# Kernel tuning notes

Measured on AMD Instinct MI355X. Metric: run time of the kernel, lower is better.

The kernel has to match this reference:

```python
import jax, jax.numpy as jnp
import numpy as np

B, T, I, H = 64, 512, 1024, 1024


def setup_inputs() -> dict:
    key = jax.random.key(0)
    ks = jax.random.split(key, 8)
    s = 0.02
    return {
        "x": jax.random.normal(ks[0], (B, T, I), dtype=jnp.float32),
        "h_0": jax.random.normal(ks[1], (B, H), dtype=jnp.float32),
        "W_ih": jax.random.normal(ks[2], (H, I), dtype=jnp.float32) * s,
        "b_ih": jax.random.normal(ks[3], (H,), dtype=jnp.float32) * s,
        "W_hh1": jax.random.normal(ks[4], (H, H), dtype=jnp.float32) * s,
        "b_hh1": jax.random.normal(ks[5], (H,), dtype=jnp.float32) * s,
        "W_hh2": jax.random.normal(ks[6], (H, H), dtype=jnp.float32) * s,
        "b_hh2": jax.random.normal(ks[7], (H,), dtype=jnp.float32) * s,
    }


def reference(x, h_0, W_ih, b_ih, W_hh1, b_hh1, W_hh2, b_hh2):
    # Shared input projection is time-independent: hoist out of the scan.
    # xp: [B, T, H]
    xp = jnp.einsum("bti,hi->bth", x, W_ih) + b_ih

    def step(h, xp_t):
        # xp_t: [B, H], h: [B, H]
        v1 = jnp.tanh(xp_t + h @ W_hh1.T + b_hh1)
        v2 = jnp.tanh(xp_t + h @ W_hh2.T + b_hh2)
        h_new = (1.0 - h) * v1 + h * v2
        return h_new, h_new

    h_T, ys = jax.lax.scan(step, h_0, jnp.swapaxes(xp, 0, 1))  # ys: [T, B, H]
    out = jnp.swapaxes(ys, 0, 1)  # [B, T, H]
    # nn.Dropout is identity in eval mode; reference is deterministic.
    return out, h_T
```

## Files before the change

kernel.cpp:

```cpp
#include <hip/hip_runtime.h>

using u32 = unsigned int;
using u64 = unsigned long long;
using bf16x8 = __attribute__((ext_vector_type(8))) short;
using f32x4  = __attribute__((ext_vector_type(4))) float;

#define BB_ 64
#define TT_ 512
#define II_ 1024
#define HH_ 1024
#define NSCAN_BLOCKS 128

__device__ __forceinline__ unsigned short bf16rne(float f) {
  u32 u = __float_as_uint(f);
  return (unsigned short)((u + 0x7FFFu + ((u >> 16) & 1u)) >> 16);
}
__device__ __forceinline__ u32 pk2(float a, float b) {
  u32 ua = __float_as_uint(a), ub = __float_as_uint(b);
  u32 lo = (ua + 0x7FFFu + ((ua >> 16) & 1u)) >> 16;
  u32 hi = (ub + 0x7FFFu + ((ub >> 16) & 1u)) & 0xFFFF0000u;
  return lo | hi;
}
__device__ __forceinline__ void gll16(const void* g, void* s) {
  __builtin_amdgcn_global_load_lds(
      (const __attribute__((address_space(1))) u32*)g,
      (__attribute__((address_space(3))) u32*)s, 16, 0, 0);
}
__device__ __forceinline__ float tanhfast(float x) {
  float e = __builtin_amdgcn_exp2f(x * 2.885390081777927f);
  return 1.0f - 2.0f / (e + 1.0f);
}

__device__ __forceinline__ void cvt4(const float* __restrict__ s, unsigned short* __restrict__ d, long long g) {
  float4 v = ((const float4*)s)[g];
  ushort4 o;
  o.x = bf16rne(v.x); o.y = bf16rne(v.y); o.z = bf16rne(v.z); o.w = bf16rne(v.w);
  ((ushort4*)d)[g] = o;
}

__global__ void k_convert(const float* __restrict__ x, const float* __restrict__ h0,
                          const float* __restrict__ Wih, const float* __restrict__ Wh1,
                          const float* __restrict__ Wh2,
                          unsigned short* __restrict__ xb, unsigned short* __restrict__ Wihb,
                          unsigned short* __restrict__ Wcatb, unsigned short* __restrict__ hbuf,
                          int* __restrict__ cnt, int do_x) {
  const long long NWI = (long long)HH_ * II_ / 4;
  const long long NH0 = (long long)BB_ * HH_ / 4;
  const long long NC  = 1024;
  const long long NX  = do_x ? ((long long)BB_ * TT_ * II_ / 4) : 0;
  const long long total = 3 * NWI + NH0 + NC + NX;
  for (long long g = (long long)blockIdx.x * blockDim.x + threadIdx.x; g < total;
       g += (long long)gridDim.x * blockDim.x) {
    if (g < NWI) {
      cvt4(Wih, Wihb, g);
    } else if (g < 2 * NWI) {
      cvt4(Wh1, Wcatb, g - NWI);
    } else if (g < 3 * NWI) {
      cvt4(Wh2, Wcatb + (long long)HH_ * II_, g - 2 * NWI);
    } else if (g < 3 * NWI + NH0) {
      cvt4(h0, hbuf, g - 3 * NWI);
    } else if (g < 3 * NWI + NH0 + NC) {
      ((int4*)cnt)[g - 3 * NWI - NH0] = make_int4(0, 0, 0, 0);
    } else {
      cvt4(x, xb, g - (3 * NWI + NH0 + NC));
    }
  }
}

template <bool XB>
__global__ __launch_bounds__(256) void k_gemm(const unsigned short* __restrict__ xbg,
                                              const float* __restrict__ xf,
                                              const unsigned short* __restrict__ Wb,
                                              const float* __restrict__ bias,
                                              float* __restrict__ C) {
  __shared__ __align__(16) unsigned short ldsA[128 * 64];
  __shared__ __align__(16) unsigned short ldsB[128 * 64];
  const int tid = threadIdx.x;
  const int w = tid >> 6, l = tid & 63;
  const int lr = l & 15, lk = l >> 4;
  const int n0 = (blockIdx.x & 7) * 128;
  const int m0 = (blockIdx.x >> 3) * 128;
  const int mbase = (w >> 1) * 64, nbase = (w & 1) * 64;

  f32x4 acc[4][4] = {};

  for (int kb = 0; kb < 16; ++kb) {
    const int k0 = kb * 64;
#pragma unroll
    for (int r = 0; r < 4; ++r) {
      int tb = r * 4096 + w * 1024 + l * 16;
      int row = tb >> 7;
      int p = (tb >> 4) & 7;
      int c = p ^ (row & 7);
      gll16(Wb + (u64)(n0 + row) * II_ + k0 + c * 8,
            (char*)ldsB + r * 4096 + w * 1024);
    }
    if constexpr (XB) {
#pragma unroll
      for (int r = 0; r < 4; ++r) {
        int tb = r * 4096 + w * 1024 + l * 16;
        int row = tb >> 7;
        int p = (tb >> 4) & 7;
        int c = p ^ (row & 7);
        gll16(xbg + (u64)(m0 + row) * II_ + k0 + c * 8,
              (char*)ldsA + r * 4096 + w * 1024);
      }
    } else {
      const int r = tid >> 1, ch = tid & 1;
      const float* gs = xf + (u64)(m0 + r) * II_ + k0 + ch * 32;
      float4 v[8];
#pragma unroll
      for (int q = 0; q < 8; ++q) v[q] = ((const float4*)gs)[q];
#pragma unroll
      for (int q = 0; q < 4; ++q) {
        int c = ch * 4 + q;
        int p = c ^ (r & 7);
        uint4 pk;
        pk.x = pk2(v[2 * q].x, v[2 * q].y);
        pk.y = pk2(v[2 * q].z, v[2 * q].w);
        pk.z = pk2(v[2 * q + 1].x, v[2 * q + 1].y);
        pk.w = pk2(v[2 * q + 1].z, v[2 * q + 1].w);
        *(uint4*)((char*)ldsA + r * 128 + p * 16) = pk;
      }
    }
    __syncthreads();

    bf16x8 a[4][2], b[4][2];
#pragma unroll
    for (int mt = 0; mt < 4; ++mt) {
      int row = mbase + mt * 16 + lr;
#pragma unroll
      for (int kk = 0; kk < 2; ++kk) {
        int c = kk * 4 + lk, p = c ^ (row & 7);
        a[mt][kk] = *(const bf16x8*)((const char*)ldsA + row * 128 + p * 16);
      }
    }
#pragma unroll
    for (int nt = 0; nt < 4; ++nt) {
      int row = nbase + nt * 16 + lr;
#pragma unroll
      for (int kk = 0; kk < 2; ++kk) {
        int c = kk * 4 + lk, p = c ^ (row & 7);
        b[nt][kk] = *(const bf16x8*)((const char*)ldsB + row * 128 + p * 16);
      }
    }
#pragma unroll
    for (int kk = 0; kk < 2; ++kk)
#pragma unroll
      for (int mt = 0; mt < 4; ++mt)
#pragma unroll
        for (int nt = 0; nt < 4; ++nt)
          acc[mt][nt] = __builtin_amdgcn_mfma_f32_16x16x32_bf16(a[mt][kk], b[nt][kk], acc[mt][nt], 0, 0, 0);
    __syncthreads();
  }

  float bn[4];
#pragma unroll
  for (int nt = 0; nt < 4; ++nt) bn[nt] = bias[n0 + nbase + nt * 16 + lr];
#pragma unroll
  for (int mt = 0; mt < 4; ++mt) {
#pragma unroll
    for (int i = 0; i < 4; ++i) {
      int m = m0 + mbase + mt * 16 + lk * 4 + i;
      float* cr = C + (u64)m * HH_ + n0 + nbase + lr;
#pragma unroll
      for (int nt = 0; nt < 4; ++nt) cr[nt * 16] = acc[mt][nt][i] + bn[nt];
    }
  }
}

__global__ __launch_bounds__(256, 1) void k_scan(float* __restrict__ out, const float* __restrict__ h0,
                                                 const float* __restrict__ b1, const float* __restrict__ b2,
                                                 const unsigned short* __restrict__ Wcat,
                                                 unsigned short* __restrict__ hbuf, u32* __restrict__ flags) {
  __shared__ float part[16 * 4 * 65];
  const int tid = threadIdx.x, w = tid >> 6, l = tid & 63;
  const int lr = l & 15, lk = l >> 4;
  const int og = blockIdx.x & 31, bg = blockIdx.x >> 5;
  const int jb = og * 32, bb = bg * 16;
  const int koff = w * 256;

  bf16x8 wt[4][8];
#pragma unroll
  for (int nt = 0; nt < 4; ++nt) {
    int nrow = (nt < 2) ? (jb + nt * 16 + lr) : (HH_ + jb + (nt - 2) * 16 + lr);
    const unsigned short* wr = Wcat + (u64)nrow * HH_ + koff + lk * 8;
#pragma unroll
    for (int kk = 0; kk < 8; ++kk) wt[nt][kk] = *(const bf16x8*)(wr + kk * 32);
  }

  const int b = tid & 15, jp = tid >> 4;
  const int grow = bb + b;
  const int c0 = jb + jp * 2;
  float bv1[2] = {b1[c0], b1[c0 + 1]};
  float bv2[2] = {b2[c0], b2[c0 + 1]};
  float hold[2] = {h0[(u64)grow * HH_ + c0], h0[(u64)grow * HH_ + c0 + 1]};
  float* outp = out + (u64)grow * TT_ * HH_ + c0;

  u32* dflag = flags + bg * 512;
  const u64 ldw = ((u64)(bb + lr) * HH_ + koff + lk * 8) >> 2;
  const u64 stw = ((u64)grow * HH_ + c0) >> 1;

  for (int t = 0; t < TT_; ++t) {
    float2 xpv = *(const float2*)(outp + (u64)t * HH_);

    if (t > 0) {
      if (w == 0) {
        const u32 need = (u32)t;
        while (true) {
          u32 v = (l < 32)
                      ? __hip_atomic_load(dflag + l * 16, __ATOMIC_RELAXED, __HIP_MEMORY_SCOPE_AGENT)
                      : 0xFFFFFFFFu;
          if (__all((int)(v >= need))) break;
        }
      }
      __syncthreads();
    }

    const u64* hB = (const u64*)hbuf + (u64)(t & 1) * (BB_ * HH_ / 4) + ldw;
    bf16x8 av[8];
#pragma unroll
    for (int kk = 0; kk < 8; ++kk) {
      union { u64 q[2]; bf16x8 v; } au;
      au.q[0] = __hip_atomic_load(hB + kk * 8,     __ATOMIC_RELAXED, __HIP_MEMORY_SCOPE_AGENT);
      au.q[1] = __hip_atomic_load(hB + kk * 8 + 1, __ATOMIC_RELAXED, __HIP_MEMORY_SCOPE_AGENT);
      av[kk] = au.v;
    }

    f32x4 acc[4] = {};
#pragma unroll
    for (int kk = 0; kk < 8; ++kk)
#pragma unroll
      for (int nt = 0; nt < 4; ++nt)
        asm("v_mfma_f32_16x16x32_bf16 %0, %1, %2, %0"
            : "+v"(acc[nt]) : "v"(av[kk]), "a"(wt[nt][kk]));
    asm volatile("s_nop 7\n\ts_nop 7\n\ts_nop 7"
                 : "+v"(acc[0]), "+v"(acc[1]), "+v"(acc[2]), "+v"(acc[3]));

#pragma unroll
    for (int nt = 0; nt < 4; ++nt)
#pragma unroll
      for (int i = 0; i < 4; ++i)
        part[((w * 4 + nt) * 4 + i) * 65 + l] = acc[nt][i];
    __syncthreads();

    float hn[2];
#pragma unroll
    for (int q = 0; q < 2; ++q) {
      const int cl = jp * 2 + q;
      const int nt1 = cl >> 4, jl = cl & 15;
      const int lidx = (b >> 2) * 16 + jl, ridx = b & 3;
      float v1 = 0.f, v2 = 0.f;
#pragma unroll
      for (int ww = 0; ww < 4; ++ww) {
        v1 += part[((ww * 4 + nt1) * 4 + ridx) * 65 + lidx];
        v2 += part[((ww * 4 + 2 + nt1) * 4 + ridx) * 65 + lidx];
      }
      float xi = (q == 0) ? xpv.x : xpv.y;
      float t1 = tanhfast(v1 + xi + bv1[q]);
      float t2 = tanhfast(v2 + xi + bv2[q]);
      hn[q] = t1 + hold[q] * (t2 - t1);
      hold[q] = hn[q];
    }

    if (t < TT_ - 1) {
      u32 wd = (u32)bf16rne(hn[0]) | ((u32)bf16rne(hn[1]) << 16);
      __hip_atomic_store((u32*)hbuf + (u64)((t + 1) & 1) * (BB_ * HH_ / 2) + stw, wd,
                         __ATOMIC_RELAXED, __HIP_MEMORY_SCOPE_AGENT);
      asm volatile("s_waitcnt vmcnt(0)" ::: "memory");
      __syncthreads();
      if (tid == 0)
        __hip_atomic_store(dflag + og * 16, (u32)(t + 1), __ATOMIC_RELAXED, __HIP_MEMORY_SCOPE_AGENT);
    } else {
      *(float2*)(out + (u64)BB_ * TT_ * HH_ + (u64)grow * HH_ + c0) = make_float2(hn[0], hn[1]);
    }

    *(float2*)(outp + (u64)t * HH_) = make_float2(hn[0], hn[1]);
  }
}

extern "C" void kernel_launch(void* const* d_in, const int* in_sizes, int n_in,
                              void* d_out, int out_size, void* d_ws, size_t ws_size,
                              hipStream_t stream) {
  const float* x    = (const float*)d_in[0];
  const float* h0   = (const float*)d_in[1];
  const float* Wih  = (const float*)d_in[2];
  const float* bih  = (const float*)d_in[3];
  const float* Whh1 = (const float*)d_in[4];
  const float* bhh1 = (const float*)d_in[5];
  const float* Whh2 = (const float*)d_in[6];
  const float* bhh2 = (const float*)d_in[7];
  float* out = (float*)d_out;

  char* ws = (char*)d_ws;
  unsigned short* Wihb  = (unsigned short*)(ws + 0);
  unsigned short* Wcatb = (unsigned short*)(ws + 2097152);
  unsigned short* hbuf  = (unsigned short*)(ws + 6291456);
  int*            cnt   = (int*)(ws + 6553600);
  unsigned short* xb    = (unsigned short*)(ws + 6569984);
  const bool fastx = ws_size >= 73678848ULL;

  hipLaunchKernelGGL(k_convert, dim3(2048), dim3(256), 0, stream,
                     x, h0, Wih, Whh1, Whh2, xb, Wihb, Wcatb, hbuf, cnt, (int)fastx);
  if (fastx)
    hipLaunchKernelGGL((k_gemm<true>), dim3(2048), dim3(256), 0, stream,
                       xb, (const float*)nullptr, Wihb, bih, out);
  else
    hipLaunchKernelGGL((k_gemm<false>), dim3(2048), dim3(256), 0, stream,
                       (const unsigned short*)nullptr, x, Wihb, bih, out);
  hipLaunchKernelGGL(k_scan, dim3(NSCAN_BLOCKS), dim3(256), 0, stream,
                     out, h0, bhh1, bhh2, Wcatb, hbuf, (u32*)cnt);
}
```

Measured before the change: 2.187 ms.

## Fuse input-projection GEMM and recurrent scan into one persistent kernel with chunk flags

Merges the input-projection GEMM and the sequential scan into one launch. The first 128 blocks run the scan and the rest run GEMM tiles, which are reordered so that time chunks of 128 steps finish in order. Each finished tile bumps a per-chunk counter, and scan blocks spin on that counter before consuming a chunk, so the recurrence can start while later projections are still being computed. The separate bf16 conversion of x is dropped in favour of converting fp32 x inside the GEMM. The risk is that GEMM blocks compete with scan blocks for compute units and memory bandwidth, and that correctness depends on the scan blocks being resident first.

Measured after the change: 2.270 ms. 3.8% more time.

```diff
diff --git a/kernel.cpp b/kernel.cpp
--- a/kernel.cpp
+++ b/kernel.cpp
@@ -9,7 +9,9 @@
 #define TT_ 512
 #define II_ 1024
 #define HH_ 1024
-#define NSCAN_BLOCKS 128
+#define SCAN_BLOCKS 128
+#define GEMM_BLOCKS 2048
+#define XP_PER_CHUNK 512u
 
 __device__ __forceinline__ unsigned short bf16rne(float f) {
   u32 u = __float_as_uint(f);
@@ -38,17 +40,16 @@
   ((ushort4*)d)[g] = o;
 }
 
-__global__ void k_convert(const float* __restrict__ x, const float* __restrict__ h0,
+__global__ void k_convert(const float* __restrict__ h0,
                           const float* __restrict__ Wih, const float* __restrict__ Wh1,
                           const float* __restrict__ Wh2,
-                          unsigned short* __restrict__ xb, unsigned short* __restrict__ Wihb,
+                          unsigned short* __restrict__ Wihb,
                           unsigned short* __restrict__ Wcatb, unsigned short* __restrict__ hbuf,
-                          int* __restrict__ cnt, int do_x) {
+                          int* __restrict__ cnt) {
   const long long NWI = (long long)HH_ * II_ / 4;
   const long long NH0 = (long long)BB_ * HH_ / 4;
   const long long NC  = 1024;
-  const long long NX  = do_x ? ((long long)BB_ * TT_ * II_ / 4) : 0;
-  const long long total = 3 * NWI + NH0 + NC + NX;
+  const long long total = 3 * NWI + NH0 + NC;
   for (long long g = (long long)blockIdx.x * blockDim.x + threadIdx.x; g < total;
        g += (long long)gridDim.x * blockDim.x) {
     if (g < NWI) {
@@ -59,27 +60,26 @@
       cvt4(Wh2, Wcatb + (long long)HH_ * II_, g - 2 * NWI);
     } else if (g < 3 * NWI + NH0) {
       cvt4(h0, hbuf, g - 3 * NWI);
-    } else if (g < 3 * NWI + NH0 + NC) {
+    } else {
       ((int4*)cnt)[g - 3 * NWI - NH0] = make_int4(0, 0, 0, 0);
-    } else {
-      cvt4(x, xb, g - (3 * NWI + NH0 + NC));
-    }
-  }
-}
-
-template <bool XB>
-__global__ __launch_bounds__(256) void k_gemm(const unsigned short* __restrict__ xbg,
-                                              const float* __restrict__ xf,
-                                              const unsigned short* __restrict__ Wb,
-                                              const float* __restrict__ bias,
-                                              float* __restrict__ C) {
-  __shared__ __align__(16) unsigned short ldsA[128 * 64];
-  __shared__ __align__(16) unsigned short ldsB[128 * 64];
+    }
+  }
+}
+
+__device__ void gemm_role(int gb, char* smem, const float* __restrict__ xf,
+                          const unsigned short* __restrict__ Wb,
+                          const float* __restrict__ bias, float* __restrict__ C,
+                          u32* __restrict__ cnt_xp) {
+  unsigned short* ldsA = (unsigned short*)smem;
+  unsigned short* ldsB = (unsigned short*)(smem + 16384);
   const int tid = threadIdx.x;
   const int w = tid >> 6, l = tid & 63;
   const int lr = l & 15, lk = l >> 4;
-  const int n0 = (blockIdx.x & 7) * 128;
-  const int m0 = (blockIdx.x >> 3) * 128;
+  const int tile = gb >> 3;
+  const int n0 = (gb & 7) * 128;
+  const int tq = tile >> 6;
+  const int bidx = tile & 63;
+  const int m0 = (bidx * 4 + tq) * 128;
   const int mbase = (w >> 1) * 64, nbase = (w & 1) * 64;
 
   f32x4 acc[4][4] = {};
@@ -95,17 +95,7 @@
       gll16(Wb + (u64)(n0 + row) * II_ + k0 + c * 8,
             (char*)ldsB + r * 4096 + w * 1024);
     }
-    if constexpr (XB) {
-#pragma unroll
-      for (int r = 0; r < 4; ++r) {
-        int tb = r * 4096 + w * 1024 + l * 16;
-        int row = tb >> 7;
-        int p = (tb >> 4) & 7;
-        int c = p ^ (row & 7);
-        gll16(xbg + (u64)(m0 + row) * II_ + k0 + c * 8,
-              (char*)ldsA + r * 4096 + w * 1024);
-      }
-    } else {
+    {
       const int r = tid >> 1, ch = tid & 1;
       const float* gs = xf + (u64)(m0 + r) * II_ + k0 + ch * 32;
       float4 v[8];
@@ -167,16 +157,23 @@
       for (int nt = 0; nt < 4; ++nt) cr[nt * 16] = acc[mt][nt][i] + bn[nt];
     }
   }
-}
-
-__global__ __launch_bounds__(256, 1) void k_scan(float* __restrict__ out, const float* __restrict__ h0,
-                                                 const float* __restrict__ b1, const float* __restrict__ b2,
-                                                 const unsigned short* __restrict__ Wcat,
-                                                 unsigned short* __restrict__ hbuf, u32* __restrict__ flags) {
-  __shared__ float part[16 * 4 * 65];
+
+  asm volatile("s_waitcnt vmcnt(0)" ::: "memory");
+  __syncthreads();
+  if (tid == 0)
+    __hip_atomic_fetch_add(cnt_xp + tq, 1u, __ATOMIC_RELEASE, __HIP_MEMORY_SCOPE_AGENT);
+}
+
+__device__ void scan_role(int sb, char* smem, float* __restrict__ out,
+                          const float* __restrict__ h0,
+                          const float* __restrict__ b1, const float* __restrict__ b2,
+                          const unsigned short* __restrict__ Wcat,
+                          unsigned short* __restrict__ hbuf, u32* __restrict__ flags,
+                          u32* __restrict__ cnt_xp) {
+  float* part = (float*)smem;
   const int tid = threadIdx.x, w = tid >> 6, l = tid & 63;
   const int lr = l & 15, lk = l >> 4;
-  const int og = blockIdx.x & 31, bg = blockIdx.x >> 5;
+  const int og = sb & 31, bg = sb >> 5;
   const int jb = og * 32, bb = bg * 16;
   const int koff = w * 256;
 
@@ -202,6 +199,11 @@
   const u64 stw = ((u64)grow * HH_ + c0) >> 1;
 
   for (int t = 0; t < TT_; ++t) {
+    if ((t & 127) == 0) {
+      while (__hip_atomic_load(cnt_xp + (t >> 7), __ATOMIC_RELAXED, __HIP_MEMORY_SCOPE_AGENT) < XP_PER_CHUNK)
+        __builtin_amdgcn_s_sleep(2);
+    }
+
     float2 xpv = *(const float2*)(outp + (u64)t * HH_);
 
     if (t > 0) {
@@ -277,6 +279,24 @@
 
     *(float2*)(outp + (u64)t * HH_) = make_float2(hn[0], hn[1]);
   }
+}
+
+__global__ __launch_bounds__(256, 1) void k_fused(float* __restrict__ out,
+                                                  const float* __restrict__ x,
+                                                  const float* __restrict__ h0,
+                                                  const float* __restrict__ bih,
+                                                  const float* __restrict__ b1,
+                                                  const float* __restrict__ b2,
+                                                  const unsigned short* __restrict__ Wihb,
+                                                  const unsigned short* __restrict__ Wcat,
+                                                  unsigned short* __restrict__ hbuf,
+                                                  u32* __restrict__ flags,
+                                                  u32* __restrict__ cnt_xp) {
+  __shared__ __align__(16) char smem[32768];
+  if (blockIdx.x < SCAN_BLOCKS)
+    scan_role(blockIdx.x, smem, out, h0, b1, b2, Wcat, hbuf, flags, cnt_xp);
+  else
+    gemm_role(blockIdx.x - SCAN_BLOCKS, smem, x, Wihb, bih, out, cnt_xp);
 }
 
 extern "C" void kernel_launch(void* const* d_in, const int* in_sizes, int n_in,
@@ -297,17 +317,11 @@
   unsigned short* Wcatb = (unsigned short*)(ws + 2097152);
   unsigned short* hbuf  = (unsigned short*)(ws + 6291456);
   int*            cnt   = (int*)(ws + 6553600);
-  unsigned short* xb    = (unsigned short*)(ws + 6569984);
-  const bool fastx = ws_size >= 73678848ULL;
-
-  hipLaunchKernelGGL(k_convert, dim3(2048), dim3(256), 0, stream,
-                     x, h0, Wih, Whh1, Whh2, xb, Wihb, Wcatb, hbuf, cnt, (int)fastx);
-  if (fastx)
-    hipLaunchKernelGGL((k_gemm<true>), dim3(2048), dim3(256), 0, stream,
-                       xb, (const float*)nullptr, Wihb, bih, out);
-  else
-    hipLaunchKernelGGL((k_gemm<false>), dim3(2048), dim3(256), 0, stream,
-                       (const unsigned short*)nullptr, x, Wihb, bih, out);
-  hipLaunchKernelGGL(k_scan, dim3(NSCAN_BLOCKS), dim3(256), 0, stream,
-                     out, h0, bhh1, bhh2, Wcatb, hbuf, (u32*)cnt);
-}
+  u32*            flags = (u32*)cnt;
+  u32*            cnt_xp = flags + 2048;
+
+  hipLaunchKernelGGL(k_convert, dim3(1024), dim3(256), 0, stream,
+                     h0, Wih, Whh1, Whh2, Wihb, Wcatb, hbuf, cnt);
+  hipLaunchKernelGGL(k_fused, dim3(SCAN_BLOCKS + GEMM_BLOCKS), dim3(256), 0, stream,
+                     out, x, h0, bih, bhh1, bhh2, Wihb, Wcatb, hbuf, flags, cnt_xp);
+}
```
